# Kernel tuning notes

Measured on AMD Instinct MI355X. Metric: run time of the kernel, lower is better.

## Reference

```python
import jax, jax.numpy as jnp
import numpy as np

B, L, D = 4, 128, 256
EPS = 1e-5

def setup_inputs() -> dict:
    key = jax.random.key(0)
    k1, k2, k3, k4, k5 = jax.random.split(key, 5)
    query = jax.random.normal(k1, (B, L, D), dtype=jnp.float32)
    value = jax.random.normal(k2, (B, L, D), dtype=jnp.float32)
    mask = jax.random.randint(k3, (B, L), 0, 2, dtype=jnp.int32)
    mask = mask.at[:, 0].set(1)  # guarantee at least one valid key per row (avoid all -inf softmax)
    norm3_w = jax.random.normal(k4, (2 * D,), dtype=jnp.float32) * 0.02 + 1.0
    norm3_b = jax.random.normal(k5, (2 * D,), dtype=jnp.float32) * 0.02
    return {"query": query, "value": value, "mask": mask, "norm3_w": norm3_w, "norm3_b": norm3_b}

def reference(query, value, mask, norm3_w, norm3_b):
    # final_queryer[b,i,j,d] = (query[b,i,d] + value[b,j,d]) / 2  -- replaces the eye-matrix expansion
    fq = (query[:, :, None, :] + value[:, None, :, :]) * 0.5          # [B,L,L,D]
    # scores over key axis k against value / query banks
    w = jnp.einsum('bijd,bkd->bijk', fq, value)                        # [B,L,L,L]
    wq = jnp.einsum('bijd,bkd->bijk', fq, query)                       # [B,L,L,L]
    keymask = (mask == 0)[:, None, None, :]                            # [B,1,1,L]
    neg_inf = jnp.float32(-jnp.inf)
    w = jnp.where(keymask, neg_inf, w)
    wq = jnp.where(keymask, neg_inf, wq)
    attn = jax.nn.softmax(w, axis=3)
    attn_q = jax.nn.softmax(wq, axis=3)
    merged = jnp.einsum('bijk,bkd->bijd', attn, value)                 # [B,L,L,D]
    merged_q = jnp.einsum('bijk,bkd->bijd', attn_q, query)             # [B,L,L,D]
    merged = jnp.concatenate([merged, merged_q], axis=-1)              # [B,L,L,2D]
    # LayerNorm over last dim (2D)
    mu = jnp.mean(merged, axis=-1, keepdims=True)
    var = jnp.mean((merged - mu) ** 2, axis=-1, keepdims=True)
    merged = (merged - mu) * jax.lax.rsqrt(var + EPS) * norm3_w + norm3_b
    # re-mask along the i axis
    merged = merged * mask[:, :, None, None].astype(merged.dtype)
    return merged
```

## Files before the change

kernel.cpp:

```cpp
#include <hip/hip_runtime.h>
#include <hip/hip_bf16.h>
#include <stdint.h>

#define BDIM 4
#define LDIM 128
#define DDIM 256
#define CDIM 512
#define EPSLN 1e-5f
#define NE (BDIM * LDIM * LDIM)
#define SROW 516

typedef float f32x4 __attribute__((ext_vector_type(4)));
typedef short s16x8 __attribute__((ext_vector_type(8)));
typedef int i32x4 __attribute__((ext_vector_type(4)));

__device__ __forceinline__ unsigned short f2bf(float f) {
    unsigned u = __builtin_bit_cast(unsigned, f);
    u += 0x7fffu + ((u >> 16) & 1u);
    return (unsigned short)(u >> 16);
}

__device__ __forceinline__ unsigned pk_bf16(float a, float b) {
    union { __hip_bfloat162 h; unsigned u; } cv;
    cv.h = __float22bfloat162_rn(make_float2(a, b));
    return cv.u;
}

__global__ __launch_bounds__(128) void k_prep(const float* __restrict__ query,
                                              const float* __restrict__ value,
                                              const int* __restrict__ mask,
                                              float* __restrict__ Es,
                                              unsigned short* __restrict__ Qt16,
                                              unsigned short* __restrict__ Vt16) {
    __shared__ __align__(16) char smem[16 * 260 * 4 + 128 * 68 * 4];
    float (*X_s)[260] = (float (*)[260])smem;
    float (*Y_s)[68] = (float (*)[68])(smem + 16 * 260 * 4);
    float (*tile)[33] = (float (*)[33])smem;

    const int t = threadIdx.x;

    if (blockIdx.z >= 4) {
        const int z2 = blockIdx.z - 4;
        const int b = z2 & 3, sel = z2 >> 2;
        const int d0 = blockIdx.x * 32, k0 = blockIdx.y * 32;
        const float* src = sel ? query : value;
        unsigned short* dst16 = sel ? Qt16 : Vt16;
        const int tx = t & 31, ty = t >> 5;
#pragma unroll
        for (int jj = 0; jj < 8; ++jj) {
            int r = ty + jj * 4;
            tile[r][tx] = src[((size_t)(b * LDIM + k0 + r)) * DDIM + d0 + tx];
        }
        __syncthreads();
#pragma unroll
        for (int jj = 0; jj < 8; ++jj) {
            int r = ty + jj * 4;
            size_t o = ((size_t)(b * DDIM + d0 + r)) * LDIM + k0 + tx;
            dst16[o] = f2bf(tile[tx][r]);
        }
        return;
    }

    const int b = blockIdx.z, which = blockIdx.y, it = blockIdx.x;
    const float* X = (which == 0 || which == 2) ? query : value;
    const float* Y = (which <= 1) ? value : query;
    const float* Xb = X + (size_t)b * LDIM * DDIM;
    const float* Yb = Y + (size_t)b * LDIM * DDIM;

    const int i0 = it * 16;
    const int iq = (t >> 5) << 2;
    const int kl = t & 31;

#pragma unroll
    for (int u = 0; u < 8; ++u) {
        int ch = u * 128 + t;
        int row = ch >> 6;
        int cc = (ch & 63) << 2;
        *(f32x4*)&X_s[row][cc] = *(const f32x4*)(Xb + (size_t)(i0 + row) * DDIM + cc);
    }

    float acc[4][4] = {};
#pragma unroll 1
    for (int ct = 0; ct < 4; ++ct) {
#pragma unroll
        for (int u = 0; u < 16; ++u) {
            int ch = u * 128 + t;
            int row = ch >> 4;
            int cc = (ch & 15) << 2;
            *(f32x4*)&Y_s[row][cc] = *(const f32x4*)(Yb + (size_t)row * DDIM + ct * 64 + cc);
        }
        __syncthreads();
#pragma unroll
        for (int u = 0; u < 16; ++u) {
            const int c = u * 4;
            f32x4 xv[4], yv[4];
#pragma unroll
            for (int ii = 0; ii < 4; ++ii) xv[ii] = *(const f32x4*)&X_s[iq + ii][ct * 64 + c];
#pragma unroll
            for (int kk = 0; kk < 4; ++kk) yv[kk] = *(const f32x4*)&Y_s[kl + 32 * kk][c];
#pragma unroll
            for (int ii = 0; ii < 4; ++ii)
#pragma unroll
                for (int kk = 0; kk < 4; ++kk)
#pragma unroll
                    for (int e = 0; e < 4; ++e)
                        acc[ii][kk] += xv[ii][e] * yv[kk][e];
        }
        __syncthreads();
    }

    int mk[4];
#pragma unroll
    for (int kk = 0; kk < 4; ++kk) mk[kk] = mask[b * LDIM + kl + 32 * kk];

    float* Eg = Es + (size_t)which * NE + (size_t)b * (LDIM * LDIM);
#pragma unroll
    for (int ii = 0; ii < 4; ++ii) {
        float lg[4];
        float mx = -3.0e38f;
#pragma unroll
        for (int kk = 0; kk < 4; ++kk) {
            lg[kk] = 0.5f * acc[ii][kk];
            if (mk[kk] != 0) mx = fmaxf(mx, lg[kk]);
        }
#pragma unroll
        for (int o = 16; o >= 1; o >>= 1) mx = fmaxf(mx, __shfl_xor(mx, o, 64));
#pragma unroll
        for (int kk = 0; kk < 4; ++kk)
            Eg[(size_t)(i0 + iq + ii) * LDIM + kl + 32 * kk] =
                (mk[kk] != 0) ? __expf(lg[kk] - mx) : 0.0f;
    }
}

__global__ __launch_bounds__(256, 2) void k_main(const float* __restrict__ E1,
                                                 const unsigned short* __restrict__ Vt16,
                                                 const unsigned short* __restrict__ Qt16,
                                                 const int* __restrict__ mask,
                                                 const float* __restrict__ nw,
                                                 const float* __restrict__ nb,
                                                 float* __restrict__ out) {
    __shared__ __align__(16) char smem[32 * SROW * 4];
    unsigned short (*P_s)[136] = (unsigned short (*)[136])smem;
    unsigned short (*Pq_s)[136] = (unsigned short (*)[136])(smem + 32 * 136 * 2);
    float (*stage)[SROW] = (float (*)[SROW])smem;
    __shared__ float wln[CDIM], bln[CDIM];
    __shared__ float zinv_s[64];
    __shared__ float maskv[32];

    const int tid = threadIdx.x;
    const int i0 = blockIdx.x * 32;
    const int j = blockIdx.y;
    const int b = blockIdx.z;

    const int lane = tid & 63;
    const int q = lane >> 4;
    const int l15 = lane & 15;
    const int wv = tid >> 6;
    const int path = wv >> 1;
    const int nh = wv & 1;

    const float* E2 = E1 + NE;
    const float* E1q = E1 + 2 * NE;
    const float* E2q = E1 + 3 * NE;

    wln[tid] = nw[tid]; wln[tid + 256] = nw[tid + 256];
    bln[tid] = nb[tid]; bln[tid + 256] = nb[tid + 256];
    if (tid < 32) maskv[tid] = (mask[b * LDIM + i0 + tid] != 0) ? 1.0f : 0.0f;

    const unsigned short* bsrc = (path ? Qt16 : Vt16) +
                                 (size_t)b * DDIM * LDIM + (size_t)(nh * 128) * LDIM;
    s16x8 bfr[8][4];
#pragma unroll
    for (int nt = 0; nt < 8; ++nt)
#pragma unroll
        for (int kc = 0; kc < 4; ++kc)
            bfr[nt][kc] = *(const s16x8*)(bsrc + (size_t)(nt * 16 + l15) * LDIM + kc * 32 + q * 8);

    {
        const int m = tid >> 3;
        const int k0 = (tid & 7) * 16;
        const float* e1 = E1 + ((size_t)(b * LDIM + i0 + m)) * LDIM + k0;
        const float* e1q = E1q + ((size_t)(b * LDIM + i0 + m)) * LDIM + k0;
        const float* e2 = E2 + ((size_t)(b * LDIM + j)) * LDIM + k0;
        const float* e2q = E2q + ((size_t)(b * LDIM + j)) * LDIM + k0;
        union { unsigned u32[8]; s16x8 v[2]; } tp, tq;
        float s = 0.f, sq = 0.f;
#pragma unroll
        for (int u4 = 0; u4 < 16; u4 += 4) {
            f32x4 a = *(const f32x4*)(e1 + u4);
            f32x4 c = *(const f32x4*)(e2 + u4);
            f32x4 aq = *(const f32x4*)(e1q + u4);
            f32x4 cq = *(const f32x4*)(e2q + u4);
            float p0 = a[0] * c[0], p1 = a[1] * c[1], p2 = a[2] * c[2], p3 = a[3] * c[3];
            float q0 = aq[0] * cq[0], q1 = aq[1] * cq[1], q2 = aq[2] * cq[2], q3 = aq[3] * cq[3];
            s += (p0 + p1) + (p2 + p3);
            sq += (q0 + q1) + (q2 + q3);
            tp.u32[u4 / 2] = pk_bf16(p0, p1);
            tp.u32[u4 / 2 + 1] = pk_bf16(p2, p3);
            tq.u32[u4 / 2] = pk_bf16(q0, q1);
            tq.u32[u4 / 2 + 1] = pk_bf16(q2, q3);
        }
        *(s16x8*)&P_s[m][k0] = tp.v[0];
        *(s16x8*)&P_s[m][k0 + 8] = tp.v[1];
        *(s16x8*)&Pq_s[m][k0] = tq.v[0];
        *(s16x8*)&Pq_s[m][k0 + 8] = tq.v[1];
        s += __shfl_xor(s, 1, 64); s += __shfl_xor(s, 2, 64); s += __shfl_xor(s, 4, 64);
        sq += __shfl_xor(sq, 1, 64); sq += __shfl_xor(sq, 2, 64); sq += __shfl_xor(sq, 4, 64);
        if ((tid & 7) == 0) { zinv_s[m] = 1.0f / s; zinv_s[32 + m] = 1.0f / sq; }
    }
    __syncthreads();

    f32x4 acc[2][8];
#pragma unroll
    for (int mt = 0; mt < 2; ++mt)
#pragma unroll
        for (int nt = 0; nt < 8; ++nt) acc[mt][nt] = (f32x4){0.f, 0.f, 0.f, 0.f};

    const unsigned short(*As)[136] = path ? Pq_s : P_s;
#pragma unroll
    for (int kc = 0; kc < 4; ++kc) {
        const s16x8 a0 = *(const s16x8*)&As[l15][kc * 32 + q * 8];
        const s16x8 a1 = *(const s16x8*)&As[16 + l15][kc * 32 + q * 8];
#pragma unroll
        for (int nt = 0; nt < 8; ++nt) {
            acc[0][nt] = __builtin_amdgcn_mfma_f32_16x16x32_bf16(a0, bfr[nt][kc], acc[0][nt], 0, 0, 0);
            acc[1][nt] = __builtin_amdgcn_mfma_f32_16x16x32_bf16(a1, bfr[nt][kc], acc[1][nt], 0, 0, 0);
        }
    }
    __syncthreads();

#pragma unroll
    for (int mt = 0; mt < 2; ++mt) {
#pragma unroll
        for (int reg = 0; reg < 4; ++reg) {
            const int row = mt * 16 + q * 4 + reg;
            const float zv = zinv_s[path * 32 + row];
#pragma unroll
            for (int nt = 0; nt < 8; ++nt) {
                const int c = path * 256 + nh * 128 + nt * 16 + l15;
                stage[row][c] = acc[mt][nt][reg] * zv;
            }
        }
    }
    __syncthreads();

    {
        const f32x4 w0 = *(const f32x4*)&wln[lane * 4];
        const f32x4 b0 = *(const f32x4*)&bln[lane * 4];
        const f32x4 w1 = *(const f32x4*)&wln[256 + lane * 4];
        const f32x4 b1 = *(const f32x4*)&bln[256 + lane * 4];
#pragma unroll
        for (int rr = 0; rr < 8; ++rr) {
            const int row = wv * 8 + rr;
            const f32x4 v0 = *(const f32x4*)&stage[row][lane * 4];
            const f32x4 v1 = *(const f32x4*)&stage[row][256 + lane * 4];
            float s1 = (v0[0] + v0[1]) + (v0[2] + v0[3]) + (v1[0] + v1[1]) + (v1[2] + v1[3]);
            float s2 = (v0[0] * v0[0] + v0[1] * v0[1]) + (v0[2] * v0[2] + v0[3] * v0[3]) +
                       (v1[0] * v1[0] + v1[1] * v1[1]) + (v1[2] * v1[2] + v1[3] * v1[3]);
#pragma unroll
            for (int o = 1; o <= 32; o <<= 1) {
                s1 += __shfl_xor(s1, o, 64);
                s2 += __shfl_xor(s2, o, 64);
            }
            const float mean = s1 * (1.0f / 512.0f);
            const float var = s2 * (1.0f / 512.0f) - mean * mean;
            const float rstd = rsqrtf(var + EPSLN);
            const float mf = maskv[row];
            float* orow = out + (((size_t)(b * LDIM + i0 + row)) * LDIM + j) * CDIM;
            f32x4 o0, o1;
#pragma unroll
            for (int u = 0; u < 4; ++u) {
                o0[u] = ((v0[u] - mean) * rstd * w0[u] + b0[u]) * mf;
                o1[u] = ((v1[u] - mean) * rstd * w1[u] + b1[u]) * mf;
            }
            *(f32x4*)&orow[lane * 4] = o0;
            *(f32x4*)&orow[256 + lane * 4] = o1;
        }
    }
}

extern "C" void kernel_launch(void* const* d_in, const int* in_sizes, int n_in,
                              void* d_out, int out_size, void* d_ws, size_t ws_size,
                              hipStream_t stream) {
    const float* query = (const float*)d_in[0];
    const float* value = (const float*)d_in[1];
    const int* mask = (const int*)d_in[2];
    const float* nw = (const float*)d_in[3];
    const float* nb = (const float*)d_in[4];
    float* out = (float*)d_out;

    char* ws = (char*)d_ws;
    const size_t NT = (size_t)BDIM * DDIM * LDIM;

    float* Es = (float*)ws;
    unsigned short* Vt16 = (unsigned short*)(ws + 4 * (size_t)NE * 4);
    unsigned short* Qt16 = Vt16 + NT;

    k_prep<<<dim3(8, 4, 12), 128, 0, stream>>>(query, value, mask, Es, Qt16, Vt16);
    k_main<<<dim3(4, 128, 4), 256, 0, stream>>>(Es, Vt16, Qt16, mask, nw, nb, out);
}
```

Baseline: 193.2 us.

## Halve row tile to 16, split B-fragment loads, fuse LayerNorm stats into epilogue

Each block now handles 16 query rows instead of 32, which doubles the grid and halves shared memory. The B fragments are loaded in two halves so fewer registers are live, and the launch bound is raised to 3 blocks per CU. The LayerNorm sums are now accumulated while the MFMA results are written to the staging buffer and reduced through a small shared array, which removes the full-row shuffle reduction. The intent is more occupancy and latency hiding for this output-write-bound kernel. In exchange, each block reloads the B matrix for half as many rows, and the split loads put a global load between the MFMA phases.

```diff
diff --git a/kernel.cpp b/kernel.cpp
--- a/kernel.cpp
+++ b/kernel.cpp
@@ -132,23 +132,24 @@
     }
 }
 
-__global__ __launch_bounds__(256, 2) void k_main(const float* __restrict__ E1,
+__global__ __launch_bounds__(256, 3) void k_main(const float* __restrict__ E1,
                                                  const unsigned short* __restrict__ Vt16,
                                                  const unsigned short* __restrict__ Qt16,
                                                  const int* __restrict__ mask,
                                                  const float* __restrict__ nw,
                                                  const float* __restrict__ nb,
                                                  float* __restrict__ out) {
-    __shared__ __align__(16) char smem[32 * SROW * 4];
+    __shared__ __align__(16) char smem[16 * SROW * 4];
     unsigned short (*P_s)[136] = (unsigned short (*)[136])smem;
-    unsigned short (*Pq_s)[136] = (unsigned short (*)[136])(smem + 32 * 136 * 2);
+    unsigned short (*Pq_s)[136] = (unsigned short (*)[136])(smem + 16 * 136 * 2);
     float (*stage)[SROW] = (float (*)[SROW])smem;
     __shared__ float wln[CDIM], bln[CDIM];
-    __shared__ float zinv_s[64];
-    __shared__ float maskv[32];
+    __shared__ float zinv_s[32];
+    __shared__ __align__(16) float red[16][4][2];
+    __shared__ float maskv[16];
 
     const int tid = threadIdx.x;
-    const int i0 = blockIdx.x * 32;
+    const int i0 = blockIdx.x * 16;
     const int j = blockIdx.y;
     const int b = blockIdx.z;
 
@@ -165,28 +166,28 @@
 
     wln[tid] = nw[tid]; wln[tid + 256] = nw[tid + 256];
     bln[tid] = nb[tid]; bln[tid + 256] = nb[tid + 256];
-    if (tid < 32) maskv[tid] = (mask[b * LDIM + i0 + tid] != 0) ? 1.0f : 0.0f;
+    if (tid < 16) maskv[tid] = (mask[b * LDIM + i0 + tid] != 0) ? 1.0f : 0.0f;
 
     const unsigned short* bsrc = (path ? Qt16 : Vt16) +
                                  (size_t)b * DDIM * LDIM + (size_t)(nh * 128) * LDIM;
-    s16x8 bfr[8][4];
+    s16x8 bfr[8][2];
 #pragma unroll
     for (int nt = 0; nt < 8; ++nt)
 #pragma unroll
-        for (int kc = 0; kc < 4; ++kc)
+        for (int kc = 0; kc < 2; ++kc)
             bfr[nt][kc] = *(const s16x8*)(bsrc + (size_t)(nt * 16 + l15) * LDIM + kc * 32 + q * 8);
 
     {
-        const int m = tid >> 3;
-        const int k0 = (tid & 7) * 16;
+        const int m = tid >> 4;
+        const int k0 = (tid & 15) * 8;
         const float* e1 = E1 + ((size_t)(b * LDIM + i0 + m)) * LDIM + k0;
         const float* e1q = E1q + ((size_t)(b * LDIM + i0 + m)) * LDIM + k0;
         const float* e2 = E2 + ((size_t)(b * LDIM + j)) * LDIM + k0;
         const float* e2q = E2q + ((size_t)(b * LDIM + j)) * LDIM + k0;
-        union { unsigned u32[8]; s16x8 v[2]; } tp, tq;
+        union { unsigned u32[4]; s16x8 v; } tp, tq;
         float s = 0.f, sq = 0.f;
 #pragma unroll
-        for (int u4 = 0; u4 < 16; u4 += 4) {
+        for (int u4 = 0; u4 < 8; u4 += 4) {
             f32x4 a = *(const f32x4*)(e1 + u4);
             f32x4 c = *(const f32x4*)(e2 + u4);
             f32x4 aq = *(const f32x4*)(e1q + u4);
@@ -200,47 +201,64 @@
             tq.u32[u4 / 2] = pk_bf16(q0, q1);
             tq.u32[u4 / 2 + 1] = pk_bf16(q2, q3);
         }
-        *(s16x8*)&P_s[m][k0] = tp.v[0];
-        *(s16x8*)&P_s[m][k0 + 8] = tp.v[1];
-        *(s16x8*)&Pq_s[m][k0] = tq.v[0];
-        *(s16x8*)&Pq_s[m][k0 + 8] = tq.v[1];
-        s += __shfl_xor(s, 1, 64); s += __shfl_xor(s, 2, 64); s += __shfl_xor(s, 4, 64);
-        sq += __shfl_xor(sq, 1, 64); sq += __shfl_xor(sq, 2, 64); sq += __shfl_xor(sq, 4, 64);
-        if ((tid & 7) == 0) { zinv_s[m] = 1.0f / s; zinv_s[32 + m] = 1.0f / sq; }
+        *(s16x8*)&P_s[m][k0] = tp.v;
+        *(s16x8*)&Pq_s[m][k0] = tq.v;
+        s += __shfl_xor(s, 1, 64); s += __shfl_xor(s, 2, 64);
+        s += __shfl_xor(s, 4, 64); s += __shfl_xor(s, 8, 64);
+        sq += __shfl_xor(sq, 1, 64); sq += __shfl_xor(sq, 2, 64);
+        sq += __shfl_xor(sq, 4, 64); sq += __shfl_xor(sq, 8, 64);
+        if ((tid & 15) == 0) { zinv_s[m] = 1.0f / s; zinv_s[16 + m] = 1.0f / sq; }
     }
     __syncthreads();
 
-    f32x4 acc[2][8];
-#pragma unroll
-    for (int mt = 0; mt < 2; ++mt)
-#pragma unroll
-        for (int nt = 0; nt < 8; ++nt) acc[mt][nt] = (f32x4){0.f, 0.f, 0.f, 0.f};
+    f32x4 acc[8];
+#pragma unroll
+    for (int nt = 0; nt < 8; ++nt) acc[nt] = (f32x4){0.f, 0.f, 0.f, 0.f};
 
     const unsigned short(*As)[136] = path ? Pq_s : P_s;
-#pragma unroll
-    for (int kc = 0; kc < 4; ++kc) {
-        const s16x8 a0 = *(const s16x8*)&As[l15][kc * 32 + q * 8];
-        const s16x8 a1 = *(const s16x8*)&As[16 + l15][kc * 32 + q * 8];
+    {
+        s16x8 a0 = *(const s16x8*)&As[l15][0 * 32 + q * 8];
+        s16x8 a1 = *(const s16x8*)&As[l15][1 * 32 + q * 8];
+#pragma unroll
+        for (int nt = 0; nt < 8; ++nt)
+            acc[nt] = __builtin_amdgcn_mfma_f32_16x16x32_bf16(a0, bfr[nt][0], acc[nt], 0, 0, 0);
+#pragma unroll
+        for (int nt = 0; nt < 8; ++nt)
+            acc[nt] = __builtin_amdgcn_mfma_f32_16x16x32_bf16(a1, bfr[nt][1], acc[nt], 0, 0, 0);
+#pragma unroll
+        for (int nt = 0; nt < 8; ++nt)
+#pragma unroll
+            for (int kc = 0; kc < 2; ++kc)
+                bfr[nt][kc] = *(const s16x8*)(bsrc + (size_t)(nt * 16 + l15) * LDIM +
+                                              (kc + 2) * 32 + q * 8);
+        s16x8 a2 = *(const s16x8*)&As[l15][2 * 32 + q * 8];
+        s16x8 a3 = *(const s16x8*)&As[l15][3 * 32 + q * 8];
+#pragma unroll
+        for (int nt = 0; nt < 8; ++nt)
+            acc[nt] = __builtin_amdgcn_mfma_f32_16x16x32_bf16(a2, bfr[nt][0], acc[nt], 0, 0, 0);
+#pragma unroll
+        for (int nt = 0; nt < 8; ++nt)
+            acc[nt] = __builtin_amdgcn_mfma_f32_16x16x32_bf16(a3, bfr[nt][1], acc[nt], 0, 0, 0);
+    }
+    __syncthreads();
+
+#pragma unroll
+    for (int reg = 0; reg < 4; ++reg) {
+        const int row = q * 4 + reg;
+        const float zv = zinv_s[path * 16 + row];
+        float s1 = 0.f, s2 = 0.f;
 #pragma unroll
         for (int nt = 0; nt < 8; ++nt) {
-            acc[0][nt] = __builtin_amdgcn_mfma_f32_16x16x32_bf16(a0, bfr[nt][kc], acc[0][nt], 0, 0, 0);
-            acc[1][nt] = __builtin_amdgcn_mfma_f32_16x16x32_bf16(a1, bfr[nt][kc], acc[1][nt], 0, 0, 0);
-        }
-    }
-    __syncthreads();
-
-#pragma unroll
-    for (int mt = 0; mt < 2; ++mt) {
-#pragma unroll
-        for (int reg = 0; reg < 4; ++reg) {
-            const int row = mt * 16 + q * 4 + reg;
-            const float zv = zinv_s[path * 32 + row];
-#pragma unroll
-            for (int nt = 0; nt < 8; ++nt) {
-                const int c = path * 256 + nh * 128 + nt * 16 + l15;
-                stage[row][c] = acc[mt][nt][reg] * zv;
-            }
-        }
+            const int c = path * 256 + nh * 128 + nt * 16 + l15;
+            const float v = acc[nt][reg] * zv;
+            stage[row][c] = v;
+            s1 += v; s2 += v * v;
+        }
+        s1 += __shfl_xor(s1, 1, 64); s2 += __shfl_xor(s2, 1, 64);
+        s1 += __shfl_xor(s1, 2, 64); s2 += __shfl_xor(s2, 2, 64);
+        s1 += __shfl_xor(s1, 4, 64); s2 += __shfl_xor(s2, 4, 64);
+        s1 += __shfl_xor(s1, 8, 64); s2 += __shfl_xor(s2, 8, 64);
+        if (l15 == 0) { red[row][wv][0] = s1; red[row][wv][1] = s2; }
     }
     __syncthreads();
 
@@ -250,22 +268,18 @@
         const f32x4 w1 = *(const f32x4*)&wln[256 + lane * 4];
         const f32x4 b1 = *(const f32x4*)&bln[256 + lane * 4];
 #pragma unroll
-        for (int rr = 0; rr < 8; ++rr) {
-            const int row = wv * 8 + rr;
+        for (int rr = 0; rr < 4; ++rr) {
+            const int row = wv * 4 + rr;
+            const f32x4 ra = *(const f32x4*)&red[row][0][0];
+            const f32x4 rb = *(const f32x4*)&red[row][2][0];
+            const float s1t = (ra[0] + ra[2]) + (rb[0] + rb[2]);
+            const float s2t = (ra[1] + ra[3]) + (rb[1] + rb[3]);
+            const float mean = s1t * (1.0f / 512.0f);
+            const float var = s2t * (1.0f / 512.0f) - mean * mean;
+            const float rstd = rsqrtf(var + EPSLN);
+            const float mf = maskv[row];
             const f32x4 v0 = *(const f32x4*)&stage[row][lane * 4];
             const f32x4 v1 = *(const f32x4*)&stage[row][256 + lane * 4];
-            float s1 = (v0[0] + v0[1]) + (v0[2] + v0[3]) + (v1[0] + v1[1]) + (v1[2] + v1[3]);
-            float s2 = (v0[0] * v0[0] + v0[1] * v0[1]) + (v0[2] * v0[2] + v0[3] * v0[3]) +
-                       (v1[0] * v1[0] + v1[1] * v1[1]) + (v1[2] * v1[2] + v1[3] * v1[3]);
-#pragma unroll
-            for (int o = 1; o <= 32; o <<= 1) {
-                s1 += __shfl_xor(s1, o, 64);
-                s2 += __shfl_xor(s2, o, 64);
-            }
-            const float mean = s1 * (1.0f / 512.0f);
-            const float var = s2 * (1.0f / 512.0f) - mean * mean;
-            const float rstd = rsqrtf(var + EPSLN);
-            const float mf = maskv[row];
             float* orow = out + (((size_t)(b * LDIM + i0 + row)) * LDIM + j) * CDIM;
             f32x4 o0, o1;
 #pragma unroll
@@ -297,5 +311,5 @@
     unsigned short* Qt16 = Vt16 + NT;
 
     k_prep<<<dim3(8, 4, 12), 128, 0, stream>>>(query, value, mask, Es, Qt16, Vt16);
-    k_main<<<dim3(4, 128, 4), 256, 0, stream>>>(Es, Vt16, Qt16, mask, nw, nb, out);
-}
+    k_main<<<dim3(8, 128, 4), 256, 0, stream>>>(Es, Vt16, Qt16, mask, nw, nb, out);
+}
```

Result: slower. 212.8 us (+10.2%).

## Fuse LayerNorm stats into MFMA epilogue and shrink prep row tiles

Applied to the files above, without the earlier changes.

The k_main epilogue now accumulates per-row sum and sum-of-squares while writing accumulators to shared staging. It reduces them across the 16 lanes with shuffles and stores per-wave partials in a small shared array, so the LayerNorm pass only reads four partials instead of doing a full 64-lane shuffle reduction per row. Separately, k_prep processes 8 query rows per block instead of 16, doubling the number of score blocks for more parallelism. The transpose blocks are re-indexed to fit the new grid. This costs extra shared memory and some redundant Y tile loads in k_prep.

```diff
diff --git a/kernel.cpp b/kernel.cpp
--- a/kernel.cpp
+++ b/kernel.cpp
@@ -32,17 +32,19 @@
                                               float* __restrict__ Es,
                                               unsigned short* __restrict__ Qt16,
                                               unsigned short* __restrict__ Vt16) {
-    __shared__ __align__(16) char smem[16 * 260 * 4 + 128 * 68 * 4];
+    __shared__ __align__(16) char smem[8 * 260 * 4 + 128 * 68 * 4];
     float (*X_s)[260] = (float (*)[260])smem;
-    float (*Y_s)[68] = (float (*)[68])(smem + 16 * 260 * 4);
+    float (*Y_s)[68] = (float (*)[68])(smem + 8 * 260 * 4);
     float (*tile)[33] = (float (*)[33])smem;
 
     const int t = threadIdx.x;
 
     if (blockIdx.z >= 4) {
-        const int z2 = blockIdx.z - 4;
-        const int b = z2 & 3, sel = z2 >> 2;
-        const int d0 = blockIdx.x * 32, k0 = blockIdx.y * 32;
+        const int idx = (blockIdx.z - 4) * 64 + blockIdx.y * 16 + blockIdx.x;
+        const int sel = idx >> 7;
+        const int b = (idx >> 5) & 3;
+        const int d0 = ((idx >> 2) & 7) * 32;
+        const int k0 = (idx & 3) * 32;
         const float* src = sel ? query : value;
         unsigned short* dst16 = sel ? Qt16 : Vt16;
         const int tx = t & 31, ty = t >> 5;
@@ -67,19 +69,19 @@
     const float* Xb = X + (size_t)b * LDIM * DDIM;
     const float* Yb = Y + (size_t)b * LDIM * DDIM;
 
-    const int i0 = it * 16;
-    const int iq = (t >> 5) << 2;
+    const int i0 = it * 8;
+    const int iq = (t >> 5) * 2;
     const int kl = t & 31;
 
 #pragma unroll
-    for (int u = 0; u < 8; ++u) {
+    for (int u = 0; u < 4; ++u) {
         int ch = u * 128 + t;
         int row = ch >> 6;
         int cc = (ch & 63) << 2;
         *(f32x4*)&X_s[row][cc] = *(const f32x4*)(Xb + (size_t)(i0 + row) * DDIM + cc);
     }
 
-    float acc[4][4] = {};
+    float acc[2][4] = {};
 #pragma unroll 1
     for (int ct = 0; ct < 4; ++ct) {
 #pragma unroll
@@ -93,13 +95,13 @@
 #pragma unroll
         for (int u = 0; u < 16; ++u) {
             const int c = u * 4;
-            f32x4 xv[4], yv[4];
-#pragma unroll
-            for (int ii = 0; ii < 4; ++ii) xv[ii] = *(const f32x4*)&X_s[iq + ii][ct * 64 + c];
+            f32x4 xv[2], yv[4];
+#pragma unroll
+            for (int ii = 0; ii < 2; ++ii) xv[ii] = *(const f32x4*)&X_s[iq + ii][ct * 64 + c];
 #pragma unroll
             for (int kk = 0; kk < 4; ++kk) yv[kk] = *(const f32x4*)&Y_s[kl + 32 * kk][c];
 #pragma unroll
-            for (int ii = 0; ii < 4; ++ii)
+            for (int ii = 0; ii < 2; ++ii)
 #pragma unroll
                 for (int kk = 0; kk < 4; ++kk)
 #pragma unroll
@@ -115,7 +117,7 @@
 
     float* Eg = Es + (size_t)which * NE + (size_t)b * (LDIM * LDIM);
 #pragma unroll
-    for (int ii = 0; ii < 4; ++ii) {
+    for (int ii = 0; ii < 2; ++ii) {
         float lg[4];
         float mx = -3.0e38f;
 #pragma unroll
@@ -145,6 +147,7 @@
     float (*stage)[SROW] = (float (*)[SROW])smem;
     __shared__ float wln[CDIM], bln[CDIM];
     __shared__ float zinv_s[64];
+    __shared__ __align__(16) float red[32][4][2];
     __shared__ float maskv[32];
 
     const int tid = threadIdx.x;
@@ -235,11 +238,19 @@
         for (int reg = 0; reg < 4; ++reg) {
             const int row = mt * 16 + q * 4 + reg;
             const float zv = zinv_s[path * 32 + row];
+            float s1 = 0.f, s2 = 0.f;
 #pragma unroll
             for (int nt = 0; nt < 8; ++nt) {
                 const int c = path * 256 + nh * 128 + nt * 16 + l15;
-                stage[row][c] = acc[mt][nt][reg] * zv;
+                const float v = acc[mt][nt][reg] * zv;
+                stage[row][c] = v;
+                s1 += v; s2 += v * v;
             }
+            s1 += __shfl_xor(s1, 1, 64); s2 += __shfl_xor(s2, 1, 64);
+            s1 += __shfl_xor(s1, 2, 64); s2 += __shfl_xor(s2, 2, 64);
+            s1 += __shfl_xor(s1, 4, 64); s2 += __shfl_xor(s2, 4, 64);
+            s1 += __shfl_xor(s1, 8, 64); s2 += __shfl_xor(s2, 8, 64);
+            if (l15 == 0) { red[row][wv][0] = s1; red[row][wv][1] = s2; }
         }
     }
     __syncthreads();
@@ -252,20 +263,16 @@
 #pragma unroll
         for (int rr = 0; rr < 8; ++rr) {
             const int row = wv * 8 + rr;
+            const f32x4 ra = *(const f32x4*)&red[row][0][0];
+            const f32x4 rb = *(const f32x4*)&red[row][2][0];
+            const float s1t = (ra[0] + ra[2]) + (rb[0] + rb[2]);
+            const float s2t = (ra[1] + ra[3]) + (rb[1] + rb[3]);
+            const float mean = s1t * (1.0f / 512.0f);
+            const float var = s2t * (1.0f / 512.0f) - mean * mean;
+            const float rstd = rsqrtf(var + EPSLN);
+            const float mf = maskv[row];
             const f32x4 v0 = *(const f32x4*)&stage[row][lane * 4];
             const f32x4 v1 = *(const f32x4*)&stage[row][256 + lane * 4];
-            float s1 = (v0[0] + v0[1]) + (v0[2] + v0[3]) + (v1[0] + v1[1]) + (v1[2] + v1[3]);
-            float s2 = (v0[0] * v0[0] + v0[1] * v0[1]) + (v0[2] * v0[2] + v0[3] * v0[3]) +
-                       (v1[0] * v1[0] + v1[1] * v1[1]) + (v1[2] * v1[2] + v1[3] * v1[3]);
-#pragma unroll
-            for (int o = 1; o <= 32; o <<= 1) {
-                s1 += __shfl_xor(s1, o, 64);
-                s2 += __shfl_xor(s2, o, 64);
-            }
-            const float mean = s1 * (1.0f / 512.0f);
-            const float var = s2 * (1.0f / 512.0f) - mean * mean;
-            const float rstd = rsqrtf(var + EPSLN);
-            const float mf = maskv[row];
             float* orow = out + (((size_t)(b * LDIM + i0 + row)) * LDIM + j) * CDIM;
             f32x4 o0, o1;
 #pragma unroll
@@ -296,6 +303,6 @@
     unsigned short* Vt16 = (unsigned short*)(ws + 4 * (size_t)NE * 4);
     unsigned short* Qt16 = Vt16 + NT;
 
-    k_prep<<<dim3(8, 4, 12), 128, 0, stream>>>(query, value, mask, Es, Qt16, Vt16);
+    k_prep<<<dim3(16, 4, 8), 128, 0, stream>>>(query, value, mask, Es, Qt16, Vt16);
     k_main<<<dim3(4, 128, 4), 256, 0, stream>>>(Es, Vt16, Qt16, mask, nw, nb, out);
 }
```

Measured after the change: 192.0 us. No clear change (-0.6%).
